# Optimization experiments

Hardware: AMD Instinct MI355X
Metric: run time of the kernel (lower is better)

The kernel has to match this reference:

```python
import jax, jax.numpy as jnp
import numpy as np

IN_F = 4096
OUT_F = 4096

def setup_inputs() -> dict:
    key = jax.random.key(0)
    k1, k2 = jax.random.split(key)
    x = jax.random.normal(k1, (8, 2048, IN_F), dtype=jnp.float32)
    weight = jax.random.normal(k2, (OUT_F, IN_F), dtype=jnp.float32) * (1.0 / IN_F ** 0.5)
    bias = jnp.zeros((OUT_F,), dtype=jnp.float32)
    return {"x": x, "weight": weight, "bias": bias}

def reference(x, weight, bias):
    # absmean scale over the full weight matrix (BitNet b1.58)
    scale = jnp.maximum(jnp.mean(jnp.abs(weight)), 1e-8)
    w_quant = jnp.clip(jnp.round(weight / scale), -1.0, 1.0)  # ternary {-1,0,+1}
    # straight-through estimator: forward uses w_quant*scale, grad flows to weight
    w_ste = jax.lax.stop_gradient(w_quant * scale - weight) + weight
    # x: [b, s, in], w_ste: [out, in] -> [b, s, out]
    return jnp.einsum('bsi,oi->bso', x, w_ste) + bias
```

## Files before the change

### kernel.cpp

```cpp
#include <hip/hip_runtime.h>
#include <stdint.h>
#include <stddef.h>

#define M_DIM 16384
#define K_DIM 4096
#define N_DIM 4096

#define BM 256
#define BN 256
#define BK 64

#define WS_SUM_OFF   0
#define WS_PART_OFF  256
#define WS_X_OFF     16384
#define WS_XBYTES    ((size_t)M_DIM * K_DIM * 2)
#define WS_W_OFF     (WS_X_OFF + WS_XBYTES)
#define WS_WBYTES    ((size_t)N_DIM * K_DIM * 2)
#define WS_NEEDED    (WS_W_OFF + WS_WBYTES)

typedef __attribute__((ext_vector_type(8))) short short8;
typedef __attribute__((ext_vector_type(4))) float floatx4;

__device__ __forceinline__ unsigned short f2bf_rne(float f) {
  unsigned u = __builtin_bit_cast(unsigned, f);
  u += 0x7FFFu + ((u >> 16) & 1u);
  return (unsigned short)(u >> 16);
}

__device__ __forceinline__ float get_scale(const double* __restrict__ sum) {
  double m = *sum * (1.0 / 16777216.0);
  return (float)fmax(m, 1e-8);
}

__device__ __forceinline__ void gload16(const void* g, void* l) {
  __builtin_amdgcn_global_load_lds(
      (const __attribute__((address_space(1))) void*)g,
      (__attribute__((address_space(3))) void*)l,
      16, 0, 0);
}

__global__ void prep_kernel(const float* __restrict__ W, double* __restrict__ partials,
                            const float* __restrict__ X, unsigned short* __restrict__ XO) {
  if (blockIdx.x < 1024) {
    const int n4 = (N_DIM * K_DIM) / 4;
    const float4* W4 = (const float4*)W;
    float s = 0.f;
    const int stride = 1024 * blockDim.x;
    for (int i = blockIdx.x * blockDim.x + threadIdx.x; i < n4; i += stride) {
      float4 v = W4[i];
      s += fabsf(v.x) + fabsf(v.y) + fabsf(v.z) + fabsf(v.w);
    }
#pragma unroll
    for (int off = 32; off > 0; off >>= 1) s += __shfl_down(s, off);
    __shared__ double bsum[4];
    if ((threadIdx.x & 63) == 0) bsum[threadIdx.x >> 6] = (double)s;
    __syncthreads();
    if (threadIdx.x == 0)
      partials[blockIdx.x] = bsum[0] + bsum[1] + bsum[2] + bsum[3];
  } else {
    const int n4 = (M_DIM * K_DIM) / 4;
    const float4* X4 = (const float4*)X;
    ushort4* O4 = (ushort4*)XO;
    const int nblk = 3072;
    const int stride = nblk * blockDim.x;
    for (int i = (blockIdx.x - 1024) * blockDim.x + threadIdx.x; i < n4; i += stride) {
      float4 v = X4[i];
      ushort4 o;
      o.x = f2bf_rne(v.x); o.y = f2bf_rne(v.y); o.z = f2bf_rne(v.z); o.w = f2bf_rne(v.w);
      O4[i] = o;
    }
  }
}

__global__ void reduce2_kernel(const double* __restrict__ partials, double* __restrict__ sum) {
  double s = 0.0;
  for (int i = threadIdx.x; i < 1024; i += 256) s += partials[i];
#pragma unroll
  for (int off = 32; off > 0; off >>= 1) s += __shfl_down(s, off);
  __shared__ double wsum[4];
  if ((threadIdx.x & 63) == 0) wsum[threadIdx.x >> 6] = s;
  __syncthreads();
  if (threadIdx.x == 0) *sum = wsum[0] + wsum[1] + wsum[2] + wsum[3];
}

__global__ void quantw_kernel(const float* __restrict__ W, const double* __restrict__ sum,
                              unsigned short* __restrict__ T) {
  const int n4 = (N_DIM * K_DIM) / 4;
  const float s = get_scale(sum);
  const float4* W4 = (const float4*)W;
  ushort4* T4 = (ushort4*)T;
  const int stride = gridDim.x * blockDim.x;
  for (int i = blockIdx.x * blockDim.x + threadIdx.x; i < n4; i += stride) {
    float4 v = W4[i];
    float q0 = fminf(fmaxf(rintf(v.x / s), -1.f), 1.f);
    float q1 = fminf(fmaxf(rintf(v.y / s), -1.f), 1.f);
    float q2 = fminf(fmaxf(rintf(v.z / s), -1.f), 1.f);
    float q3 = fminf(fmaxf(rintf(v.w / s), -1.f), 1.f);
    ushort4 o;
    o.x = f2bf_rne(q0); o.y = f2bf_rne(q1); o.z = f2bf_rne(q2); o.w = f2bf_rne(q3);
    T4[i] = o;
  }
}

__device__ __forceinline__ void stage64(const unsigned short* __restrict__ src,
                                        int gRow0, int kBase, char* ldsSlab) {
  const int t = threadIdx.x;
  const int r = t >> 3;
  const int g = (t & 7) ^ (r & 7);
  gload16(src + (size_t)(gRow0 + r) * K_DIM + kBase + (g << 3),
          ldsSlab + ((t >> 6) << 10));
}

template <int Q>
__device__ __forceinline__ void mfma_quad(floatx4 (&acc)[8][4],
                                          const short8 (&F)[2][2],
                                          const short8 (&bfr)[4][2]) {
#pragma unroll
  for (int j = 0; j < 2; ++j) {
#pragma unroll
    for (int ni = 0; ni < 4; ++ni) {
      acc[2 * Q + j][ni] = __builtin_amdgcn_mfma_f32_16x16x32_bf16(
          F[j][0], bfr[ni][0], acc[2 * Q + j][ni], 0, 0, 0);
      acc[2 * Q + j][ni] = __builtin_amdgcn_mfma_f32_16x16x32_bf16(
          F[j][1], bfr[ni][1], acc[2 * Q + j][ni], 0, 0, 0);
    }
  }
}

#define LDA(P, off) (*(const short8*)(smem + (P) * 65536 + (off)))
#define LDB(P, off) (*(const short8*)(smem + (P) * 65536 + 32768 + (off)))

#define TILE_BODY(T, P)                                                       \
  {                                                                           \
      \
    _Pragma("unroll")                                                         \
    for (int ni = 0; ni < 4; ++ni) {                                          \
      bf[ni][0] = LDB(P, bOff0 + ni * 2048);                                  \
      bf[ni][1] = LDB(P, bOff1 + ni * 2048);                                  \
    }                                                                         \
    afA[0][0] = LDA(P, aOff0);        afA[0][1] = LDA(P, aOff1);              \
    afA[1][0] = LDA(P, aOff0 + 2048); afA[1][1] = LDA(P, aOff1 + 2048);       \
    if ((T) + 1 < 64) {                                                       \
      stage64(B, blockN + 128, ((T) + 1) << 6,                                \
              smem + (1 - (P)) * 65536 + 32768 + 128 * 128);                  \
      stage64(B, blockN + 192, ((T) + 1) << 6,                                \
              smem + (1 - (P)) * 65536 + 32768 + 192 * 128);                  \
    }                                                                         \
    __builtin_amdgcn_s_barrier();                                             \
    asm volatile("s_waitcnt lgkmcnt(0)" ::: "memory");                        \
    __builtin_amdgcn_sched_barrier(0);                                        \
    __builtin_amdgcn_s_setprio(1);                                            \
    mfma_quad<0>(acc, afA, bf);                                               \
    __builtin_amdgcn_s_setprio(0);                                            \
    __builtin_amdgcn_s_barrier();                                             \
                                                               \
    afA[0][0] = LDA(P, aOff0 + 4096); afA[0][1] = LDA(P, aOff1 + 4096);       \
    afA[1][0] = LDA(P, aOff0 + 6144); afA[1][1] = LDA(P, aOff1 + 6144);       \
    if ((T) + 2 < 64) {                                                       \
      stage64(B, blockN + 0,  ((T) + 2) << 6, smem + (P) * 65536 + 32768);    \
      stage64(B, blockN + 64, ((T) + 2) << 6,                                 \
              smem + (P) * 65536 + 32768 + 64 * 128);                         \
    }                                                                         \
    __builtin_amdgcn_s_barrier();                                             \
    asm volatile("s_waitcnt lgkmcnt(0)" ::: "memory");                        \
    __builtin_amdgcn_sched_barrier(0);                                        \
    __builtin_amdgcn_s_setprio(1);                                            \
    mfma_quad<1>(acc, afA, bf);                                               \
    __builtin_amdgcn_s_setprio(0);                                            \
    __builtin_amdgcn_s_barrier();                                             \
             \
    afA[0][0] = LDA(P, aOff0 + 8192);  afA[0][1] = LDA(P, aOff1 + 8192);      \
    afA[1][0] = LDA(P, aOff0 + 10240); afA[1][1] = LDA(P, aOff1 + 10240);     \
    afB[0][0] = LDA(P, aOff0 + 12288); afB[0][1] = LDA(P, aOff1 + 12288);     \
    afB[1][0] = LDA(P, aOff0 + 14336); afB[1][1] = LDA(P, aOff1 + 14336);     \
    if ((T) + 2 < 64) {                                                       \
      stage64(A, blockM + 0,   ((T) + 2) << 6, smem + (P) * 65536);           \
      stage64(A, blockM + 128, ((T) + 2) << 6,                                \
              smem + (P) * 65536 + 128 * 128);                                \
    }                                                                         \
    __builtin_amdgcn_s_barrier();                                             \
    asm volatile("s_waitcnt lgkmcnt(0)" ::: "memory");                        \
    __builtin_amdgcn_sched_barrier(0);                                        \
    __builtin_amdgcn_s_setprio(1);                                            \
    mfma_quad<2>(acc, afA, bf);                                               \
    __builtin_amdgcn_s_setprio(0);                                            \
    __builtin_amdgcn_s_barrier();                                             \
                        \
    if ((T) + 2 < 64) {                                                       \
      stage64(A, blockM + 64,  ((T) + 2) << 6,                                \
              smem + (P) * 65536 + 64 * 128);                                 \
      stage64(A, blockM + 192, ((T) + 2) << 6,                                \
              smem + (P) * 65536 + 192 * 128);                                \
    }                                                                         \
    __builtin_amdgcn_s_barrier();                                             \
    __builtin_amdgcn_s_setprio(1);                                            \
    mfma_quad<3>(acc, afB, bf);                                               \
    __builtin_amdgcn_s_setprio(0);                                            \
    if ((T) < 62) {                                                           \
      asm volatile("s_waitcnt vmcnt(6)" ::: "memory");                        \
      __builtin_amdgcn_s_barrier();                                           \
    } else if ((T) == 62) {                                                   \
      asm volatile("s_waitcnt vmcnt(0)" ::: "memory");                        \
      __builtin_amdgcn_s_barrier();                                           \
    }                                                                         \
  }

__global__ __launch_bounds__(512, 2) void gemm_kernel(
    const unsigned short* __restrict__ A,
    const unsigned short* __restrict__ B,
    const float* __restrict__ bias,
    const double* __restrict__ sum,
    float* __restrict__ C) {
  __shared__ __align__(16) char smem[131072];

  const int tid = threadIdx.x;
  const int l = tid & 63;
  const int wid = tid >> 6;
  const int wm = wid >> 2;
  const int wn = wid & 3;

  const int lin = blockIdx.x;
  const int swz = ((lin & 7) << 7) | (lin >> 3);
  const int blockM = (swz >> 4) << 8;
  const int blockN = (swz & 15) << 8;

  const int laneRow = l & 15;
  const int c0 = (l >> 4) ^ (l & 7);
  const int aOff0 = ((wm * 128 + laneRow) * 8 + c0) << 4;
  const int aOff1 = aOff0 ^ 64;
  const int bOff0 = ((wn * 64 + laneRow) * 8 + c0) << 4;
  const int bOff1 = bOff0 ^ 64;

  floatx4 acc[8][4] = {};
  short8 bf[4][2], afA[2][2], afB[2][2];

  stage64(A, blockM + 0,   0, smem + 0);
  stage64(A, blockM + 128, 0, smem + 128 * 128);
  stage64(A, blockM + 64,  0, smem + 64 * 128);
  stage64(A, blockM + 192, 0, smem + 192 * 128);
  stage64(B, blockN + 0,   0, smem + 32768);
  stage64(B, blockN + 64,  0, smem + 32768 + 64 * 128);
  stage64(B, blockN + 128, 0, smem + 32768 + 128 * 128);
  stage64(B, blockN + 192, 0, smem + 32768 + 192 * 128);
  stage64(B, blockN + 0,   64, smem + 65536 + 32768);
  stage64(B, blockN + 64,  64, smem + 65536 + 32768 + 64 * 128);
  stage64(A, blockM + 0,   64, smem + 65536);
  stage64(A, blockM + 128, 64, smem + 65536 + 128 * 128);
  stage64(A, blockM + 64,  64, smem + 65536 + 64 * 128);
  stage64(A, blockM + 192, 64, smem + 65536 + 192 * 128);
  asm volatile("s_waitcnt vmcnt(6)" ::: "memory");
  __builtin_amdgcn_s_barrier();

  for (int tp = 0; tp < 32; ++tp) {
    const int t0 = tp * 2;
    TILE_BODY(t0, 0)
    TILE_BODY(t0 + 1, 1)
  }

  const float s = get_scale(sum);
  const int col16 = l & 15;
  const int rquad = (l >> 4) * 4;
#pragma unroll
  for (int ni = 0; ni < 4; ++ni) {
    const int col = blockN + wn * 64 + ni * 16 + col16;
    const float bv = bias[col];
#pragma unroll
    for (int mi = 0; mi < 8; ++mi) {
      const int row0 = blockM + wm * 128 + mi * 16 + rquad;
      float* Cp = C + (size_t)row0 * N_DIM + col;
#pragma unroll
      for (int r = 0; r < 4; ++r)
        Cp[(size_t)r * N_DIM] = acc[mi][ni][r] * s + bv;
    }
  }
}

extern "C" void kernel_launch(void* const* d_in, const int* in_sizes, int n_in,
                              void* d_out, int out_size, void* d_ws, size_t ws_size,
                              hipStream_t stream) {
  const float* x = (const float*)d_in[0];
  const float* wt = (const float*)d_in[1];
  const float* bias = (const float*)d_in[2];
  float* out = (float*)d_out;

  if (ws_size < WS_NEEDED) return;

  double* sum = (double*)((char*)d_ws + WS_SUM_OFF);
  double* partials = (double*)((char*)d_ws + WS_PART_OFF);
  unsigned short* xb = (unsigned short*)((char*)d_ws + WS_X_OFF);
  unsigned short* wb = (unsigned short*)((char*)d_ws + WS_W_OFF);

  prep_kernel<<<4096, 256, 0, stream>>>(wt, partials, x, xb);
  reduce2_kernel<<<1, 256, 0, stream>>>(partials, sum);
  quantw_kernel<<<1024, 256, 0, stream>>>(wt, sum, wb);
  gemm_kernel<<<1024, 512, 0, stream>>>(xb, wb, bias, sum, out);
}
```

Before: 898.0 us.

## Prefetch next tile's LDS fragments across iterations with double-buffered B registers

Restructures the GEMM main loop so the B fragments and the first half of the A fragments for the next K tile are read from LDS at the end of the current tile, into ping-pong register sets. The MFMA phases can then wait on partial lgkmcnt counts instead of draining the LDS queue. Global staging addresses become per-thread pointers advanced by BK, replacing per-call address recomputation. This raises register pressure considerably (more short8 fragments live at once), which risks spills or lower occupancy under the 512x2 launch bounds.

Result: slower. 2.087 ms (+132.4%).

```diff
diff --git a/kernel.cpp b/kernel.cpp
--- a/kernel.cpp
+++ b/kernel.cpp
@@ -102,19 +102,15 @@
   }
 }
 
-__device__ __forceinline__ void stage64(const unsigned short* __restrict__ src,
-                                        int gRow0, int kBase, char* ldsSlab) {
-  const int t = threadIdx.x;
-  const int r = t >> 3;
-  const int g = (t & 7) ^ (r & 7);
-  gload16(src + (size_t)(gRow0 + r) * K_DIM + kBase + (g << 3),
-          ldsSlab + ((t >> 6) << 10));
+__device__ __forceinline__ void stage_adv(const unsigned short*& p, char* ldsSlab) {
+  gload16(p, ldsSlab + ((threadIdx.x >> 6) << 10));
+  p += BK;
 }
 
 template <int Q>
-__device__ __forceinline__ void mfma_quad(floatx4 (&acc)[8][4],
-                                          const short8 (&F)[2][2],
-                                          const short8 (&bfr)[4][2]) {
+__device__ __forceinline__ void mfma_set(floatx4 (&acc)[8][4],
+                                         const short8 (&F)[2][2],
+                                         const short8 (&bfr)[4][2]) {
 #pragma unroll
   for (int j = 0; j < 2; ++j) {
 #pragma unroll
@@ -130,79 +126,77 @@
 #define LDA(P, off) (*(const short8*)(smem + (P) * 65536 + (off)))
 #define LDB(P, off) (*(const short8*)(smem + (P) * 65536 + 32768 + (off)))
 
-#define TILE_BODY(T, P)                                                       \
+#define TILE_BODY(T, P, BFC, BFN)                                             \
   {                                                                           \
-      \
-    _Pragma("unroll")                                                         \
-    for (int ni = 0; ni < 4; ++ni) {                                          \
-      bf[ni][0] = LDB(P, bOff0 + ni * 2048);                                  \
-      bf[ni][1] = LDB(P, bOff1 + ni * 2048);                                  \
-    }                                                                         \
-    afA[0][0] = LDA(P, aOff0);        afA[0][1] = LDA(P, aOff1);              \
-    afA[1][0] = LDA(P, aOff0 + 2048); afA[1][1] = LDA(P, aOff1 + 2048);       \
+               \
+    fC[0][0] = LDA(P, aOff0 + 8192);  fC[0][1] = LDA(P, aOff1 + 8192);        \
+    fC[1][0] = LDA(P, aOff0 + 10240); fC[1][1] = LDA(P, aOff1 + 10240);       \
     if ((T) + 1 < 64) {                                                       \
-      stage64(B, blockN + 128, ((T) + 1) << 6,                                \
-              smem + (1 - (P)) * 65536 + 32768 + 128 * 128);                  \
-      stage64(B, blockN + 192, ((T) + 1) << 6,                                \
-              smem + (1 - (P)) * 65536 + 32768 + 192 * 128);                  \
+      stage_adv(pB1a, smem + (1 - (P)) * 65536 + 32768 + 128 * 128);          \
+      stage_adv(pB1b, smem + (1 - (P)) * 65536 + 32768 + 192 * 128);          \
+    }                                                                         \
+    __builtin_amdgcn_s_barrier();                                             \
+    asm volatile("s_waitcnt lgkmcnt(4)" ::: "memory");                        \
+    __builtin_amdgcn_sched_barrier(0);                                        \
+    __builtin_amdgcn_s_setprio(1);                                            \
+    mfma_set<0>(acc, fA, BFC);                                                \
+    __builtin_amdgcn_s_setprio(0);                                            \
+    __builtin_amdgcn_s_barrier();                                             \
+                \
+    fD[0][0] = LDA(P, aOff0 + 12288); fD[0][1] = LDA(P, aOff1 + 12288);       \
+    fD[1][0] = LDA(P, aOff0 + 14336); fD[1][1] = LDA(P, aOff1 + 14336);       \
+    if ((T) + 2 < 64) {                                                       \
+      stage_adv(pB0a, smem + (P) * 65536 + 32768);                            \
+      stage_adv(pB0b, smem + (P) * 65536 + 32768 + 64 * 128);                 \
+    }                                                                         \
+    __builtin_amdgcn_s_barrier();                                             \
+    asm volatile("s_waitcnt lgkmcnt(4)" ::: "memory");                        \
+    __builtin_amdgcn_sched_barrier(0);                                        \
+    __builtin_amdgcn_s_setprio(1);                                            \
+    mfma_set<1>(acc, fB, BFC);                                                \
+    __builtin_amdgcn_s_setprio(0);                                            \
+    __builtin_amdgcn_s_barrier();                                             \
+       \
+    if ((T) + 2 < 64) {                                                       \
+      stage_adv(pA0a, smem + (P) * 65536);                                    \
+      stage_adv(pA0b, smem + (P) * 65536 + 128 * 128);                        \
     }                                                                         \
     __builtin_amdgcn_s_barrier();                                             \
     asm volatile("s_waitcnt lgkmcnt(0)" ::: "memory");                        \
     __builtin_amdgcn_sched_barrier(0);                                        \
     __builtin_amdgcn_s_setprio(1);                                            \
-    mfma_quad<0>(acc, afA, bf);                                               \
+    mfma_set<2>(acc, fC, BFC);                                                \
     __builtin_amdgcn_s_setprio(0);                                            \
-    __builtin_amdgcn_s_barrier();                                             \
-                                                               \
-    afA[0][0] = LDA(P, aOff0 + 4096); afA[0][1] = LDA(P, aOff1 + 4096);       \
-    afA[1][0] = LDA(P, aOff0 + 6144); afA[1][1] = LDA(P, aOff1 + 6144);       \
+    if ((T) == 62) {                                                          \
+      asm volatile("s_waitcnt vmcnt(0)" ::: "memory");                        \
+    } else {                                                                  \
+      asm volatile("s_waitcnt vmcnt(4)" ::: "memory");                        \
+    }                                                                         \
+    __builtin_amdgcn_s_barrier();                                             \
+        \
+    if ((T) + 1 < 64) {                                                       \
+      _Pragma("unroll")                                                       \
+      for (int ni = 0; ni < 4; ++ni) {                                        \
+        BFN[ni][0] = LDB(1 - (P), bOff0 + ni * 2048);                         \
+        BFN[ni][1] = LDB(1 - (P), bOff1 + ni * 2048);                         \
+      }                                                                       \
+      fA[0][0] = LDA(1 - (P), aOff0);        fA[0][1] = LDA(1 - (P), aOff1);  \
+      fA[1][0] = LDA(1 - (P), aOff0 + 2048);                                  \
+      fA[1][1] = LDA(1 - (P), aOff1 + 2048);                                  \
+      fB[0][0] = LDA(1 - (P), aOff0 + 4096);                                  \
+      fB[0][1] = LDA(1 - (P), aOff1 + 4096);                                  \
+      fB[1][0] = LDA(1 - (P), aOff0 + 6144);                                  \
+      fB[1][1] = LDA(1 - (P), aOff1 + 6144);                                  \
+    }                                                                         \
     if ((T) + 2 < 64) {                                                       \
-      stage64(B, blockN + 0,  ((T) + 2) << 6, smem + (P) * 65536 + 32768);    \
-      stage64(B, blockN + 64, ((T) + 2) << 6,                                 \
-              smem + (P) * 65536 + 32768 + 64 * 128);                         \
-    }                                                                         \
-    __builtin_amdgcn_s_barrier();                                             \
-    asm volatile("s_waitcnt lgkmcnt(0)" ::: "memory");                        \
-    __builtin_amdgcn_sched_barrier(0);                                        \
+      stage_adv(pA1a, smem + (P) * 65536 + 64 * 128);                         \
+      stage_adv(pA1b, smem + (P) * 65536 + 192 * 128);                        \
+    }                                                                         \
+    __builtin_amdgcn_s_barrier();                                             \
     __builtin_amdgcn_s_setprio(1);                                            \
-    mfma_quad<1>(acc, afA, bf);                                               \
+    mfma_set<3>(acc, fD, BFC);                                                \
     __builtin_amdgcn_s_setprio(0);                                            \
     __builtin_amdgcn_s_barrier();                                             \
-             \
-    afA[0][0] = LDA(P, aOff0 + 8192);  afA[0][1] = LDA(P, aOff1 + 8192);      \
-    afA[1][0] = LDA(P, aOff0 + 10240); afA[1][1] = LDA(P, aOff1 + 10240);     \
-    afB[0][0] = LDA(P, aOff0 + 12288); afB[0][1] = LDA(P, aOff1 + 12288);     \
-    afB[1][0] = LDA(P, aOff0 + 14336); afB[1][1] = LDA(P, aOff1 + 14336);     \
-    if ((T) + 2 < 64) {                                                       \
-      stage64(A, blockM + 0,   ((T) + 2) << 6, smem + (P) * 65536);           \
-      stage64(A, blockM + 128, ((T) + 2) << 6,                                \
-              smem + (P) * 65536 + 128 * 128);                                \
-    }                                                                         \
-    __builtin_amdgcn_s_barrier();                                             \
-    asm volatile("s_waitcnt lgkmcnt(0)" ::: "memory");                        \
-    __builtin_amdgcn_sched_barrier(0);                                        \
-    __builtin_amdgcn_s_setprio(1);                                            \
-    mfma_quad<2>(acc, afA, bf);                                               \
-    __builtin_amdgcn_s_setprio(0);                                            \
-    __builtin_amdgcn_s_barrier();                                             \
-                        \
-    if ((T) + 2 < 64) {                                                       \
-      stage64(A, blockM + 64,  ((T) + 2) << 6,                                \
-              smem + (P) * 65536 + 64 * 128);                                 \
-      stage64(A, blockM + 192, ((T) + 2) << 6,                                \
-              smem + (P) * 65536 + 192 * 128);                                \
-    }                                                                         \
-    __builtin_amdgcn_s_barrier();                                             \
-    __builtin_amdgcn_s_setprio(1);                                            \
-    mfma_quad<3>(acc, afB, bf);                                               \
-    __builtin_amdgcn_s_setprio(0);                                            \
-    if ((T) < 62) {                                                           \
-      asm volatile("s_waitcnt vmcnt(6)" ::: "memory");                        \
-      __builtin_amdgcn_s_barrier();                                           \
-    } else if ((T) == 62) {                                                   \
-      asm volatile("s_waitcnt vmcnt(0)" ::: "memory");                        \
-      __builtin_amdgcn_s_barrier();                                           \
-    }                                                                         \
   }
 
 __global__ __launch_bounds__(512, 2) void gemm_kernel(
@@ -231,30 +225,51 @@
   const int bOff0 = ((wn * 64 + laneRow) * 8 + c0) << 4;
   const int bOff1 = bOff0 ^ 64;
 
+  const int sr = tid >> 3;
+  const int sg = (tid & 7) ^ (sr & 7);
+  const size_t thOff = (size_t)sr * K_DIM + (sg << 3);
+  const unsigned short* pA0a = A + (size_t)(blockM + 0)   * K_DIM + thOff;
+  const unsigned short* pA0b = A + (size_t)(blockM + 128) * K_DIM + thOff;
+  const unsigned short* pA1a = A + (size_t)(blockM + 64)  * K_DIM + thOff;
+  const unsigned short* pA1b = A + (size_t)(blockM + 192) * K_DIM + thOff;
+  const unsigned short* pB0a = B + (size_t)(blockN + 0)   * K_DIM + thOff;
+  const unsigned short* pB0b = B + (size_t)(blockN + 64)  * K_DIM + thOff;
+  const unsigned short* pB1a = B + (size_t)(blockN + 128) * K_DIM + thOff;
+  const unsigned short* pB1b = B + (size_t)(blockN + 192) * K_DIM + thOff;
+
   floatx4 acc[8][4] = {};
-  short8 bf[4][2], afA[2][2], afB[2][2];
-
-  stage64(A, blockM + 0,   0, smem + 0);
-  stage64(A, blockM + 128, 0, smem + 128 * 128);
-  stage64(A, blockM + 64,  0, smem + 64 * 128);
-  stage64(A, blockM + 192, 0, smem + 192 * 128);
-  stage64(B, blockN + 0,   0, smem + 32768);
-  stage64(B, blockN + 64,  0, smem + 32768 + 64 * 128);
-  stage64(B, blockN + 128, 0, smem + 32768 + 128 * 128);
-  stage64(B, blockN + 192, 0, smem + 32768 + 192 * 128);
-  stage64(B, blockN + 0,   64, smem + 65536 + 32768);
-  stage64(B, blockN + 64,  64, smem + 65536 + 32768 + 64 * 128);
-  stage64(A, blockM + 0,   64, smem + 65536);
-  stage64(A, blockM + 128, 64, smem + 65536 + 128 * 128);
-  stage64(A, blockM + 64,  64, smem + 65536 + 64 * 128);
-  stage64(A, blockM + 192, 64, smem + 65536 + 192 * 128);
+  short8 bfE[4][2], bfO[4][2], fA[2][2], fB[2][2], fC[2][2], fD[2][2];
+
+  stage_adv(pA0a, smem + 0);
+  stage_adv(pA0b, smem + 128 * 128);
+  stage_adv(pA1a, smem + 64 * 128);
+  stage_adv(pA1b, smem + 192 * 128);
+  stage_adv(pB0a, smem + 32768);
+  stage_adv(pB0b, smem + 32768 + 64 * 128);
+  stage_adv(pB1a, smem + 32768 + 128 * 128);
+  stage_adv(pB1b, smem + 32768 + 192 * 128);
+  stage_adv(pB0a, smem + 65536 + 32768);
+  stage_adv(pB0b, smem + 65536 + 32768 + 64 * 128);
+  stage_adv(pA0a, smem + 65536);
+  stage_adv(pA0b, smem + 65536 + 128 * 128);
+  stage_adv(pA1a, smem + 65536 + 64 * 128);
+  stage_adv(pA1b, smem + 65536 + 192 * 128);
   asm volatile("s_waitcnt vmcnt(6)" ::: "memory");
   __builtin_amdgcn_s_barrier();
+#pragma unroll
+  for (int ni = 0; ni < 4; ++ni) {
+    bfE[ni][0] = LDB(0, bOff0 + ni * 2048);
+    bfE[ni][1] = LDB(0, bOff1 + ni * 2048);
+  }
+  fA[0][0] = LDA(0, aOff0);        fA[0][1] = LDA(0, aOff1);
+  fA[1][0] = LDA(0, aOff0 + 2048); fA[1][1] = LDA(0, aOff1 + 2048);
+  fB[0][0] = LDA(0, aOff0 + 4096); fB[0][1] = LDA(0, aOff1 + 4096);
+  fB[1][0] = LDA(0, aOff0 + 6144); fB[1][1] = LDA(0, aOff1 + 6144);
 
   for (int tp = 0; tp < 32; ++tp) {
     const int t0 = tp * 2;
-    TILE_BODY(t0, 0)
-    TILE_BODY(t0 + 1, 1)
+    TILE_BODY(t0, 0, bfE, bfO)
+    TILE_BODY(t0 + 1, 1, bfO, bfE)
   }
 
   const float s = get_scale(sum);
```
